# Performance work log

Hardware: AMD Instinct MI355X
Metric: run time of the kernel (lower is better)

Reference implementation:

```python
import jax, jax.numpy as jnp
import numpy as np

G, NPG = 256, 128          # graphs per batch, nodes per graph
N = G * NPG                # 32768 total nodes
E = 524288                 # total directed edges; first half 'in', second half 'out'
DIN, D = 128, 256          # input feature dim, hidden dim
R = 200                    # num relations
C = 2                      # num classes
EPS = 1e-5                 # batchnorm eps


def setup_inputs() -> dict:
    key = jax.random.key(0)
    ks = jax.random.split(key, 20)

    def w(k, shape):
        fan_in = shape[-2] if len(shape) >= 2 else shape[-1]
        return jax.random.normal(k, shape, jnp.float32) / np.float32(np.sqrt(fan_in))

    return {
        "x": jax.random.normal(ks[0], (N, DIN), jnp.float32),
        "rel_emb": w(ks[1], (R, DIN)),
        # conv1: DIN -> D
        "w_in1": w(ks[2], (DIN, D)), "w_out1": w(ks[3], (DIN, D)),
        "w_loop1": w(ks[4], (DIN, D)), "w_rel1": w(ks[5], (DIN, D)),
        "loop_rel1": w(ks[6], (1, DIN)),
        "bias1": jnp.zeros((D,), jnp.float32),
        "gamma1": jnp.ones((D,), jnp.float32), "beta1": jnp.zeros((D,), jnp.float32),
        # conv2..conv5 stacked: D -> D
        "W_in": w(ks[7], (4, D, D)), "W_out": w(ks[8], (4, D, D)),
        "W_loop": w(ks[9], (4, D, D)), "W_rel": w(ks[10], (4, D, D)),
        "Loop_rel": w(ks[11], (4, 1, D)),
        "Bias": jnp.zeros((4, D), jnp.float32),
        "Gamma": jnp.ones((4, D), jnp.float32), "Beta": jnp.zeros((4, D), jnp.float32),
        # head: concat2 => Linear(4*D, C)
        "lin_w": w(ks[12], (4 * D, C)), "lin_b": jnp.zeros((C,), jnp.float32),
        # graph data (int constants)
        "edge_index": jax.random.randint(ks[13], (2, E), 0, N),
        "edge_type": jax.random.randint(ks[14], (E,), 0, R),
        "batch": jnp.repeat(jnp.arange(G, dtype=jnp.int32), NPG),
        "rel_labels": jax.random.randint(ks[15], (G,), 0, R),
    }


def _compgcn_conv(x, rel, edge_index, edge_type,
                  w_in, w_out, w_loop, w_rel, loop_rel, bias, gamma, beta):
    """One CompGCNConv layer (opn='mult', dropout=identity/eval, BN with batch stats)."""
    n = x.shape[0]
    half = edge_index.shape[1] // 2

    def direction(idx, etype, W):
        src, dst = idx[0], idx[1]
        # symmetric normalization: deg^{-1/2}[src] * deg^{-1/2}[dst]
        deg = jax.ops.segment_sum(jnp.ones_like(src, jnp.float32), src, num_segments=n)
        dinv = jnp.where(deg > 0, deg ** -0.5, 0.0)
        norm = dinv[src] * dinv[dst]                       # [half]
        msg = ((x[src] * rel[etype]) @ W) * norm[:, None]  # [half, D]
        return jax.ops.segment_sum(msg, dst, num_segments=n)

    in_res = direction(edge_index[:, :half], edge_type[:half], w_in)
    out_res = direction(edge_index[:, half:], edge_type[half:], w_out)
    loop_res = (x * loop_rel) @ w_loop                     # self-loop, loop relation, no norm

    out = (in_res + out_res + loop_res) / 3.0 + bias
    mean = out.mean(axis=0)
    var = out.var(axis=0)
    out = (out - mean) / jnp.sqrt(var + EPS) * gamma + beta
    return jax.nn.relu(out), rel @ w_rel


def reference(x, rel_emb, w_in1, w_out1, w_loop1, w_rel1, loop_rel1, bias1, gamma1, beta1,
              W_in, W_out, W_loop, W_rel, Loop_rel, Bias, Gamma, Beta,
              lin_w, lin_b, edge_index, edge_type, batch, rel_labels):
    x, r = _compgcn_conv(x, rel_emb, edge_index, edge_type,
                         w_in1, w_out1, w_loop1, w_rel1, loop_rel1, bias1, gamma1, beta1)
    for l in range(4):  # conv2..conv5 (fixed small layer loop)
        x, r = _compgcn_conv(x, r, edge_index, edge_type,
                             W_in[l], W_out[l], W_loop[l], W_rel[l],
                             Loop_rel[l], Bias[l], Gamma[l], Beta[l])

    # per-graph head/tail nodes (first two nodes of each graph) via segment offsets
    counts = jax.ops.segment_sum(jnp.ones((x.shape[0],), jnp.float32), batch, num_segments=G)
    offsets = (jnp.cumsum(counts) - counts).astype(jnp.int32)
    h_batch = x[offsets]
    t_batch = x[offsets + 1]

    pooled = jax.ops.segment_sum(x, batch, num_segments=G) / counts[:, None]
    rel_embs = r[rel_labels]

    feats = jnp.concatenate([pooled, rel_embs, h_batch, t_batch], axis=1)  # concat2 path
    return feats @ lin_w + lin_b


if __name__ == "__main__":
    out = reference(**setup_inputs())
    print(out.shape, out.dtype)
```

## Files before the change

kernel.cpp:

```cpp
#include <hip/hip_runtime.h>

#define NN 32768
#define GG 256
#define NPGN 128
#define ET 524288
#define EH 262144
#define D1 128
#define D2 256
#define RR 200

typedef unsigned short u16;
typedef __attribute__((ext_vector_type(8))) short bf16x8;
typedef __attribute__((ext_vector_type(4))) float f32x4;
typedef __attribute__((ext_vector_type(8))) unsigned short u16x8;
typedef __attribute__((ext_vector_type(4))) unsigned short u16x4;

__device__ __forceinline__ float bf2f(u16 u) {
    union { unsigned int i; float f; } v; v.i = ((unsigned int)u) << 16; return v.f;
}
__device__ __forceinline__ u16 f2bf(float f) {
    union { unsigned int i; float f; } v; v.f = f;
    unsigned int x = v.i;
    return (u16)((x + 0x7fffu + ((x >> 16) & 1u)) >> 16);
}

__global__ void k_hist(const int* __restrict__ ei, int* __restrict__ hs_in,
                       int* __restrict__ hs_out, int* __restrict__ hd_in,
                       int* __restrict__ hd_out) {
    int e = blockIdx.x * blockDim.x + threadIdx.x;
    if (e >= ET) return;
    int s = ei[e], d = ei[ET + e];
    if (e < EH) { atomicAdd(&hs_in[s], 1);  atomicAdd(&hd_in[d], 1); }
    else        { atomicAdd(&hs_out[s], 1); atomicAdd(&hd_out[d], 1); }
}

__global__ void k_dinv(const int* __restrict__ hs_in, const int* __restrict__ hs_out,
                       float* __restrict__ dinv_in, float* __restrict__ dinv_out) {
    int n = blockIdx.x * blockDim.x + threadIdx.x;
    if (n >= NN) return;
    int a = hs_in[n], b = hs_out[n];
    dinv_in[n]  = a > 0 ? rsqrtf((float)a) : 0.f;
    dinv_out[n] = b > 0 ? rsqrtf((float)b) : 0.f;
}

__global__ __launch_bounds__(1024) void k_scan(const int* __restrict__ hist,
                                               int* __restrict__ off) {
    __shared__ int lds[1024];
    int t = threadIdx.x;
    int base = t * 32;
    int loc[32];
    int s = 0;
#pragma unroll
    for (int i = 0; i < 32; ++i) { loc[i] = s; s += hist[base + i]; }
    lds[t] = s;
    int tot = s;
    __syncthreads();
    for (int st = 1; st < 1024; st <<= 1) {
        int v = (t >= st) ? lds[t - st] : 0;
        __syncthreads();
        lds[t] += v;
        __syncthreads();
    }
    int excl = lds[t] - tot;
#pragma unroll
    for (int i = 0; i < 32; ++i) off[base + i] = excl + loc[i];
    if (t == 1023) off[NN] = lds[1023];
}

__global__ void k_fill(const int* __restrict__ ei, const int* __restrict__ et,
                       const float* __restrict__ dinv, const int* __restrict__ off,
                       int* __restrict__ cur, int* __restrict__ c_src,
                       int* __restrict__ c_et, float* __restrict__ c_norm, int eoff) {
    int e = blockIdx.x * blockDim.x + threadIdx.x;
    if (e >= EH) return;
    int s = ei[eoff + e], d = ei[ET + eoff + e], t = et[eoff + e];
    int slot = off[d] + atomicAdd(&cur[d], 1);
    c_src[slot] = s;
    c_et[slot] = t;
    c_norm[slot] = dinv[s] * dinv[d];
}

__global__ void k_convx(const float* __restrict__ in, u16* __restrict__ out, int n) {
    int i = blockIdx.x * blockDim.x + threadIdx.x;
    if (i < n) out[i] = f2bf(in[i]);
}

__global__ void k_prepw(const float* __restrict__ Wi, const float* __restrict__ Wo,
                        const float* __restrict__ Wl, const float* __restrict__ lr,
                        u16* __restrict__ WiT, u16* __restrict__ WoT,
                        u16* __restrict__ WlT, int K, int L) {
    int idx = blockIdx.x * blockDim.x + threadIdx.x;
    int per = L * K * 256;
    if (idx >= 3 * per) return;
    int fam = idx / per, rem = idx % per;
    int l = rem / (K * 256), rr = rem % (K * 256);
    int k = rr / 256, n = rr % 256;
    const float* src = fam == 0 ? Wi : fam == 1 ? Wo : Wl;
    float v = src[((size_t)l * K + k) * 256 + n];
    if (fam == 2) v *= lr[l * K + k];
    u16* dst = fam == 0 ? WiT : fam == 1 ? WoT : WlT;
    dst[((size_t)l * 256 + n) * K + k] = f2bf(v);
}

template <int K>
__global__ __launch_bounds__(256) void k_gather2(
    const u16* __restrict__ x, const u16* __restrict__ relb,
    const int* __restrict__ csI, const int* __restrict__ cetI,
    const float* __restrict__ cnI, const int* __restrict__ offI,
    const int* __restrict__ csO, const int* __restrict__ cetO,
    const float* __restrict__ cnO, const int* __restrict__ offO,
    u16* __restrict__ aggI, u16* __restrict__ aggO) {
    constexpr int VEC = K / 32;
    const int dir = blockIdx.y;
    const int* __restrict__ cs  = dir ? csO : csI;
    const int* __restrict__ cet = dir ? cetO : cetI;
    const float* __restrict__ cn = dir ? cnO : cnI;
    const int* __restrict__ off = dir ? offO : offI;
    u16* __restrict__ agg = dir ? aggO : aggI;

    int node = blockIdx.x * 8 + (threadIdx.x >> 5);
    int l = threadIdx.x & 31;
    int c = l * VEC;
    int e0 = off[node], e1 = off[node + 1];
    float acc[VEC] = {};
    int e = e0;
    for (; e + 2 <= e1; e += 2) {
        int s0 = cs[e],     t0 = cet[e];     float n0 = cn[e];
        int s1 = cs[e + 1], t1 = cet[e + 1]; float n1 = cn[e + 1];
        if constexpr (VEC == 8) {
            u16x8 x0 = *(const u16x8*)(x + (size_t)s0 * K + c);
            u16x8 r0 = *(const u16x8*)(relb + (size_t)t0 * K + c);
            u16x8 x1 = *(const u16x8*)(x + (size_t)s1 * K + c);
            u16x8 r1 = *(const u16x8*)(relb + (size_t)t1 * K + c);
#pragma unroll
            for (int i = 0; i < 8; ++i)
                acc[i] += n0 * bf2f(x0[i]) * bf2f(r0[i]) + n1 * bf2f(x1[i]) * bf2f(r1[i]);
        } else {
            u16x4 x0 = *(const u16x4*)(x + (size_t)s0 * K + c);
            u16x4 r0 = *(const u16x4*)(relb + (size_t)t0 * K + c);
            u16x4 x1 = *(const u16x4*)(x + (size_t)s1 * K + c);
            u16x4 r1 = *(const u16x4*)(relb + (size_t)t1 * K + c);
#pragma unroll
            for (int i = 0; i < 4; ++i)
                acc[i] += n0 * bf2f(x0[i]) * bf2f(r0[i]) + n1 * bf2f(x1[i]) * bf2f(r1[i]);
        }
    }
    if (e < e1) {
        int s0 = cs[e], t0 = cet[e]; float n0 = cn[e];
        if constexpr (VEC == 8) {
            u16x8 x0 = *(const u16x8*)(x + (size_t)s0 * K + c);
            u16x8 r0 = *(const u16x8*)(relb + (size_t)t0 * K + c);
#pragma unroll
            for (int i = 0; i < 8; ++i) acc[i] += n0 * bf2f(x0[i]) * bf2f(r0[i]);
        } else {
            u16x4 x0 = *(const u16x4*)(x + (size_t)s0 * K + c);
            u16x4 r0 = *(const u16x4*)(relb + (size_t)t0 * K + c);
#pragma unroll
            for (int i = 0; i < 4; ++i) acc[i] += n0 * bf2f(x0[i]) * bf2f(r0[i]);
        }
    }
    if constexpr (VEC == 8) {
        u16x8 o;
#pragma unroll
        for (int i = 0; i < 8; ++i) o[i] = f2bf(acc[i]);
        *(u16x8*)(agg + (size_t)node * K + c) = o;
    } else {
        u16x4 o;
#pragma unroll
        for (int i = 0; i < 4; ++i) o[i] = f2bf(acc[i]);
        *(u16x4*)(agg + (size_t)node * K + c) = o;
    }
}

template <int K>
__global__ __launch_bounds__(256) void k_gemm_mfma(
    const u16* __restrict__ A1, const u16* __restrict__ A2, const u16* __restrict__ A3,
    const u16* __restrict__ W1, const u16* __restrict__ W2, const u16* __restrict__ W3,
    const float* __restrict__ bias, float* __restrict__ C, float* __restrict__ bnsums) {
    const int tid = threadIdx.x;
    const int wave = tid >> 6, lane = tid & 63;
    const int q = lane >> 4, r = lane & 15;
    const int rowBase = blockIdx.x * 128 + (wave & 1) * 64;
    const int colBase = blockIdx.y * 128 + (wave >> 1) * 64;
    f32x4 zero = {0.f, 0.f, 0.f, 0.f};
    f32x4 acc[4][4];
#pragma unroll
    for (int i = 0; i < 4; ++i)
#pragma unroll
        for (int j = 0; j < 4; ++j) acc[i][j] = zero;

    const u16* As[3] = {A1, A2, A3};
    const u16* Ws[3] = {W1, W2, W3};
    constexpr int SPS = K / 32;
    constexpr int TOT = 3 * SPS;

    bf16x8 aC[4], bC[4], aN[4], bN[4];
#pragma unroll
    for (int t = 0; t < 4; ++t) {
        aC[t] = *(const bf16x8*)(As[0] + (size_t)(rowBase + t * 16 + r) * K + q * 8);
        bC[t] = *(const bf16x8*)(Ws[0] + (size_t)(colBase + t * 16 + r) * K + q * 8);
    }
#pragma unroll
    for (int s = 0; s < TOT; ++s) {
        if (s + 1 < TOT) {
            const u16* A = As[(s + 1) / SPS];
            const u16* W = Ws[(s + 1) / SPS];
            const int kb = ((s + 1) % SPS) * 32 + q * 8;
#pragma unroll
            for (int t = 0; t < 4; ++t) {
                aN[t] = *(const bf16x8*)(A + (size_t)(rowBase + t * 16 + r) * K + kb);
                bN[t] = *(const bf16x8*)(W + (size_t)(colBase + t * 16 + r) * K + kb);
            }
        }
#pragma unroll
        for (int tm = 0; tm < 4; ++tm)
#pragma unroll
            for (int tn = 0; tn < 4; ++tn)
                acc[tm][tn] = __builtin_amdgcn_mfma_f32_16x16x32_bf16(
                    aC[tm], bC[tn], acc[tm][tn], 0, 0, 0);
#pragma unroll
        for (int t = 0; t < 4; ++t) { aC[t] = aN[t]; bC[t] = bN[t]; }
    }

#pragma unroll
    for (int tn = 0; tn < 4; ++tn) {
        int col = colBase + tn * 16 + r;
        float bv = bias[col];
        float sv = 0.f, qv = 0.f;
#pragma unroll
        for (int tm = 0; tm < 4; ++tm) {
#pragma unroll
            for (int reg = 0; reg < 4; ++reg) {
                int row = rowBase + tm * 16 + q * 4 + reg;
                float v = acc[tm][tn][reg] / 3.0f + bv;
                C[(size_t)row * 256 + col] = v;
                sv += v; qv += v * v;
            }
        }
        sv += __shfl_xor(sv, 16); sv += __shfl_xor(sv, 32);
        qv += __shfl_xor(qv, 16); qv += __shfl_xor(qv, 32);
        if (q == 0) {
            atomicAdd(&bnsums[col], sv);
            atomicAdd(&bnsums[256 + col], qv);
        }
    }
}

__global__ __launch_bounds__(256) void k_gemm_rel(
    const float* __restrict__ A, const float* __restrict__ W,
    float* __restrict__ C, u16* __restrict__ Cb, int M, int K) {
    __shared__ float As[16][68];
    __shared__ float Wshm[16][68];
    const int tid = threadIdx.x;
    const int tx = tid & 15, ty = tid >> 4;
    const int arow = tid >> 2;
    const int akc  = (tid & 3) << 2;
    const int wk   = tid >> 4;
    const int wn0  = (tid & 15) << 2;
    const int rowBase = blockIdx.x << 6;
    const int colBase = blockIdx.y << 6;
    float acc[4][4] = {};
    for (int k0 = 0; k0 < K; k0 += 16) {
        float4 av = make_float4(0.f, 0.f, 0.f, 0.f);
        int rr = rowBase + arow;
        if (rr < M) av = *(const float4*)(A + (size_t)rr * K + k0 + akc);
        As[akc + 0][arow] = av.x;
        As[akc + 1][arow] = av.y;
        As[akc + 2][arow] = av.z;
        As[akc + 3][arow] = av.w;
        float4 wv = *(const float4*)(W + (size_t)(k0 + wk) * D2 + colBase + wn0);
        Wshm[wk][wn0 + 0] = wv.x;
        Wshm[wk][wn0 + 1] = wv.y;
        Wshm[wk][wn0 + 2] = wv.z;
        Wshm[wk][wn0 + 3] = wv.w;
        __syncthreads();
#pragma unroll
        for (int kk = 0; kk < 16; ++kk) {
            float a0 = As[kk][(ty << 2) + 0], a1 = As[kk][(ty << 2) + 1];
            float a2 = As[kk][(ty << 2) + 2], a3 = As[kk][(ty << 2) + 3];
            float w0 = Wshm[kk][(tx << 2) + 0], w1 = Wshm[kk][(tx << 2) + 1];
            float w2 = Wshm[kk][(tx << 2) + 2], w3 = Wshm[kk][(tx << 2) + 3];
            acc[0][0] += a0 * w0; acc[0][1] += a0 * w1; acc[0][2] += a0 * w2; acc[0][3] += a0 * w3;
            acc[1][0] += a1 * w0; acc[1][1] += a1 * w1; acc[1][2] += a1 * w2; acc[1][3] += a1 * w3;
            acc[2][0] += a2 * w0; acc[2][1] += a2 * w1; acc[2][2] += a2 * w2; acc[2][3] += a2 * w3;
            acc[3][0] += a3 * w0; acc[3][1] += a3 * w1; acc[3][2] += a3 * w2; acc[3][3] += a3 * w3;
        }
        __syncthreads();
    }
#pragma unroll
    for (int i = 0; i < 4; ++i) {
        int rr = rowBase + (ty << 2) + i;
        if (rr >= M) continue;
        float* cp = C + (size_t)rr * D2 + colBase + (tx << 2);
        u16* cb = Cb + (size_t)rr * D2 + colBase + (tx << 2);
        cp[0] = acc[i][0]; cp[1] = acc[i][1]; cp[2] = acc[i][2]; cp[3] = acc[i][3];
        cb[0] = f2bf(acc[i][0]); cb[1] = f2bf(acc[i][1]);
        cb[2] = f2bf(acc[i][2]); cb[3] = f2bf(acc[i][3]);
    }
}

__global__ void k_bnapply(const float4* __restrict__ h4, const float* __restrict__ sums,
                          const float* __restrict__ gamma, const float* __restrict__ beta,
                          u16x4* __restrict__ xb4) {
    int idx = blockIdx.x * blockDim.x + threadIdx.x;
    int f0 = (idx & 63) << 2;
    float4 v = h4[idx];
    u16x4 o;
    float vv[4] = {v.x, v.y, v.z, v.w};
#pragma unroll
    for (int i = 0; i < 4; ++i) {
        int f = f0 + i;
        float mean = sums[f] * (1.0f / NN);
        float var  = sums[256 + f] * (1.0f / NN) - mean * mean;
        float inv  = 1.0f / sqrtf(var + 1e-5f);
        float t = (vv[i] - mean) * inv * gamma[f] + beta[f];
        o[i] = f2bf(t > 0.f ? t : 0.f);
    }
    xb4[idx] = o;
}

__global__ void k_feats(const u16* __restrict__ x, const float* __restrict__ rel,
                        const int* __restrict__ rel_labels, float* __restrict__ feats) {
    int g = blockIdx.x, f = threadIdx.x;
    const u16* xg = x + (size_t)g * NPGN * D2;
    float s = 0.f;
#pragma unroll 8
    for (int n = 0; n < NPGN; ++n) s += bf2f(xg[(size_t)n * D2 + f]);
    float* fg = feats + (size_t)g * 1024;
    fg[f]       = s * (1.0f / NPGN);
    fg[256 + f] = rel[(size_t)rel_labels[g] * D2 + f];
    fg[512 + f] = bf2f(xg[f]);
    fg[768 + f] = bf2f(xg[D2 + f]);
}

__global__ void k_head(const float* __restrict__ feats, const float* __restrict__ lw,
                       const float* __restrict__ lb, float* __restrict__ out) {
    int g = blockIdx.x, t = threadIdx.x;
    __shared__ float s0[256], s1[256];
    float a0 = 0.f, a1 = 0.f;
#pragma unroll
    for (int j = 0; j < 4; ++j) {
        int k = t * 4 + j;
        float fv = feats[(size_t)g * 1024 + k];
        a0 += fv * lw[k * 2 + 0];
        a1 += fv * lw[k * 2 + 1];
    }
    s0[t] = a0; s1[t] = a1;
    __syncthreads();
    for (int s = 128; s > 0; s >>= 1) {
        if (t < s) { s0[t] += s0[t + s]; s1[t] += s1[t + s]; }
        __syncthreads();
    }
    if (t == 0) {
        out[g * 2 + 0] = s0[0] + lb[0];
        out[g * 2 + 1] = s1[0] + lb[1];
    }
}

extern "C" void kernel_launch(void* const* d_in, const int* in_sizes, int n_in,
                              void* d_out, int out_size, void* d_ws, size_t ws_size,
                              hipStream_t stream) {
    const float* x0   = (const float*)d_in[0];
    const float* rel0 = (const float*)d_in[1];
    const int* edge_index = (const int*)d_in[20];
    const int* edge_type  = (const int*)d_in[21];
    const int* rel_labels = (const int*)d_in[23];
    float* out = (float*)d_out;

    float* ws = (float*)d_ws;
    float* h     = ws;
    float* relA  = h + (size_t)NN * 256;
    float* relB  = relA + (size_t)RR * 256;
    float* dinv_in  = relB + (size_t)RR * 256;
    float* dinv_out = dinv_in + NN;
    float* cnorm_in  = dinv_out + NN;
    float* cnorm_out = cnorm_in + EH;
    float* bnsums    = cnorm_out + EH;
    float* feats     = bnsums + 512;
    int* csrc_in  = (int*)(feats + GG * 1024);
    int* cet_in   = csrc_in + EH;
    int* csrc_out = cet_in + EH;
    int* cet_out  = csrc_out + EH;
    int* off_in   = cet_out + EH;
    int* off_out  = off_in + NN + 8;
    int* hs_in    = off_out + NN + 8;
    int* hs_out   = hs_in + NN;
    int* hd_in    = hs_out + NN;
    int* hd_out   = hd_in + NN;
    int* cur_in   = hd_out + NN;
    int* cur_out  = cur_in + NN;
    u16* xbf0 = (u16*)(cur_out + NN);
    u16* xbfA = xbf0 + (size_t)NN * 128;
    u16* aggI = xbfA + (size_t)NN * 256;
    u16* aggO = aggI + (size_t)NN * 256;
    u16* wt0  = aggO + (size_t)NN * 256;
    u16* wtS  = wt0 + 3 * 256 * 128;
    u16* relbf = wtS + 12 * 65536;

    hipMemsetAsync(hs_in, 0, 6 * NN * sizeof(int), stream);
    k_hist<<<ET / 256, 256, 0, stream>>>(edge_index, hs_in, hs_out, hd_in, hd_out);
    k_dinv<<<NN / 256, 256, 0, stream>>>(hs_in, hs_out, dinv_in, dinv_out);
    k_scan<<<1, 1024, 0, stream>>>(hd_in, off_in);
    k_scan<<<1, 1024, 0, stream>>>(hd_out, off_out);
    k_fill<<<EH / 256, 256, 0, stream>>>(edge_index, edge_type, dinv_in, off_in,
                                         cur_in, csrc_in, cet_in, cnorm_in, 0);
    k_fill<<<EH / 256, 256, 0, stream>>>(edge_index, edge_type, dinv_out, off_out,
                                         cur_out, csrc_out, cet_out, cnorm_out, EH);
    k_convx<<<(NN * D1) / 256, 256, 0, stream>>>(x0, xbf0, NN * D1);
    k_convx<<<(RR * D1 + 255) / 256, 256, 0, stream>>>(rel0, relbf, RR * D1);
    k_prepw<<<(3 * D1 * 256) / 256, 256, 0, stream>>>(
        (const float*)d_in[2], (const float*)d_in[3], (const float*)d_in[4],
        (const float*)d_in[6], wt0, wt0 + 256 * D1, wt0 + 2 * 256 * D1, D1, 1);
    k_prepw<<<(3 * 4 * D2 * 256) / 256, 256, 0, stream>>>(
        (const float*)d_in[10], (const float*)d_in[11], (const float*)d_in[12],
        (const float*)d_in[14], wtS, wtS + 4 * 65536, wtS + 8 * 65536, D2, 4);

    const float* rc = rel0; float* rn = relA;

    for (int l = 0; l < 5; ++l) {
        const int K = (l == 0) ? D1 : D2;
        const u16* xb = (l == 0) ? xbf0 : xbfA;
        const u16 *WiT, *WoT, *WlT;
        const float *Wr, *bias, *gamma, *beta;
        if (l == 0) {
            WiT = wt0; WoT = wt0 + 256 * D1; WlT = wt0 + 2 * 256 * D1;
            Wr = (const float*)d_in[5];
            bias  = (const float*)d_in[7];
            gamma = (const float*)d_in[8];
            beta  = (const float*)d_in[9];
        } else {
            int m = l - 1;
            WiT = wtS + (size_t)m * 65536;
            WoT = wtS + (size_t)(4 + m) * 65536;
            WlT = wtS + (size_t)(8 + m) * 65536;
            Wr = (const float*)d_in[13] + (size_t)m * D2 * D2;
            bias  = (const float*)d_in[15] + (size_t)m * D2;
            gamma = (const float*)d_in[16] + (size_t)m * D2;
            beta  = (const float*)d_in[17] + (size_t)m * D2;
        }

        dim3 ggr(NN / 8, 2);
        if (K == D1) k_gather2<D1><<<ggr, 256, 0, stream>>>(xb, relbf, csrc_in, cet_in,
            cnorm_in, off_in, csrc_out, cet_out, cnorm_out, off_out, aggI, aggO);
        else         k_gather2<D2><<<ggr, 256, 0, stream>>>(xb, relbf, csrc_in, cet_in,
            cnorm_in, off_in, csrc_out, cet_out, cnorm_out, off_out, aggI, aggO);
        hipMemsetAsync(bnsums, 0, 512 * sizeof(float), stream);
        dim3 ggrid(NN / 128, 2);
        if (K == D1) k_gemm_mfma<D1><<<ggrid, 256, 0, stream>>>(aggI, aggO, xb, WiT, WoT, WlT, bias, h, bnsums);
        else         k_gemm_mfma<D2><<<ggrid, 256, 0, stream>>>(aggI, aggO, xb, WiT, WoT, WlT, bias, h, bnsums);
        k_bnapply<<<(NN * 256 / 4) / 256, 256, 0, stream>>>((const float4*)h, bnsums,
                                                            gamma, beta, (u16x4*)xbfA);
        k_gemm_rel<<<dim3(4, 4), 256, 0, stream>>>(rc, Wr, rn, relbf, RR, K);
        const float* nr = rn;
        rn = (l == 0) ? relB : (float*)rc;
        rc = nr;
    }

    k_feats<<<GG, 256, 0, stream>>>(xbfA, rc, rel_labels, feats);
    k_head<<<GG, 256, 0, stream>>>(feats, (const float*)d_in[18],
                                   (const float*)d_in[19], out);
}
```

Baseline: 925.8 us.

## Stage GEMM tiles through LDS with async loads and widen gather edges

The MFMA GEMM now stages 128x32 A and W tiles into double-buffered shared memory using global_load_lds, rather than each wave loading its fragments directly from global memory. This lets waves in a block reuse the same tile data and cuts redundant global traffic. The gather kernel now uses 8-wide bf16 vectors for both hidden sizes (16 nodes per block for K=128) and processes 4 edges per iteration to raise memory-level parallelism. The risks are a __syncthreads per k-step, which can stall while async loads are still in flight, and higher register pressure in the gather loop.

```diff
diff --git a/kernel.cpp b/kernel.cpp
--- a/kernel.cpp
+++ b/kernel.cpp
@@ -110,7 +110,8 @@
     const int* __restrict__ csO, const int* __restrict__ cetO,
     const float* __restrict__ cnO, const int* __restrict__ offO,
     u16* __restrict__ aggI, u16* __restrict__ aggO) {
-    constexpr int VEC = K / 32;
+    constexpr int LPN = K / 8;
+    constexpr int NPB = 256 / LPN;
     const int dir = blockIdx.y;
     const int* __restrict__ cs  = dir ? csO : csI;
     const int* __restrict__ cet = dir ? cetO : cetI;
@@ -118,57 +119,53 @@
     const int* __restrict__ off = dir ? offO : offI;
     u16* __restrict__ agg = dir ? aggO : aggI;
 
-    int node = blockIdx.x * 8 + (threadIdx.x >> 5);
-    int l = threadIdx.x & 31;
-    int c = l * VEC;
+    int node = blockIdx.x * NPB + (threadIdx.x / LPN);
+    int lane = threadIdx.x % LPN;
+    int c = lane * 8;
     int e0 = off[node], e1 = off[node + 1];
-    float acc[VEC] = {};
+    float acc[8] = {};
     int e = e0;
-    for (; e + 2 <= e1; e += 2) {
-        int s0 = cs[e],     t0 = cet[e];     float n0 = cn[e];
-        int s1 = cs[e + 1], t1 = cet[e + 1]; float n1 = cn[e + 1];
-        if constexpr (VEC == 8) {
-            u16x8 x0 = *(const u16x8*)(x + (size_t)s0 * K + c);
-            u16x8 r0 = *(const u16x8*)(relb + (size_t)t0 * K + c);
-            u16x8 x1 = *(const u16x8*)(x + (size_t)s1 * K + c);
-            u16x8 r1 = *(const u16x8*)(relb + (size_t)t1 * K + c);
-#pragma unroll
-            for (int i = 0; i < 8; ++i)
-                acc[i] += n0 * bf2f(x0[i]) * bf2f(r0[i]) + n1 * bf2f(x1[i]) * bf2f(r1[i]);
-        } else {
-            u16x4 x0 = *(const u16x4*)(x + (size_t)s0 * K + c);
-            u16x4 r0 = *(const u16x4*)(relb + (size_t)t0 * K + c);
-            u16x4 x1 = *(const u16x4*)(x + (size_t)s1 * K + c);
-            u16x4 r1 = *(const u16x4*)(relb + (size_t)t1 * K + c);
-#pragma unroll
-            for (int i = 0; i < 4; ++i)
-                acc[i] += n0 * bf2f(x0[i]) * bf2f(r0[i]) + n1 * bf2f(x1[i]) * bf2f(r1[i]);
-        }
-    }
-    if (e < e1) {
+    for (; e + 4 <= e1; e += 4) {
+        int s0 = cs[e],     s1 = cs[e + 1], s2 = cs[e + 2], s3 = cs[e + 3];
+        int t0 = cet[e],    t1 = cet[e + 1], t2 = cet[e + 2], t3 = cet[e + 3];
+        float n0 = cn[e], n1 = cn[e + 1], n2 = cn[e + 2], n3 = cn[e + 3];
+        u16x8 xa = *(const u16x8*)(x + (size_t)s0 * K + c);
+        u16x8 xb = *(const u16x8*)(x + (size_t)s1 * K + c);
+        u16x8 xc = *(const u16x8*)(x + (size_t)s2 * K + c);
+        u16x8 xd = *(const u16x8*)(x + (size_t)s3 * K + c);
+        u16x8 ra = *(const u16x8*)(relb + (size_t)t0 * K + c);
+        u16x8 rb = *(const u16x8*)(relb + (size_t)t1 * K + c);
+        u16x8 rc = *(const u16x8*)(relb + (size_t)t2 * K + c);
+        u16x8 rd = *(const u16x8*)(relb + (size_t)t3 * K + c);
+#pragma unroll
+        for (int i = 0; i < 8; ++i)
+            acc[i] += n0 * bf2f(xa[i]) * bf2f(ra[i]) + n1 * bf2f(xb[i]) * bf2f(rb[i])
+                    + n2 * bf2f(xc[i]) * bf2f(rc[i]) + n3 * bf2f(xd[i]) * bf2f(rd[i]);
+    }
+    for (; e < e1; ++e) {
         int s0 = cs[e], t0 = cet[e]; float n0 = cn[e];
-        if constexpr (VEC == 8) {
-            u16x8 x0 = *(const u16x8*)(x + (size_t)s0 * K + c);
-            u16x8 r0 = *(const u16x8*)(relb + (size_t)t0 * K + c);
-#pragma unroll
-            for (int i = 0; i < 8; ++i) acc[i] += n0 * bf2f(x0[i]) * bf2f(r0[i]);
-        } else {
-            u16x4 x0 = *(const u16x4*)(x + (size_t)s0 * K + c);
-            u16x4 r0 = *(const u16x4*)(relb + (size_t)t0 * K + c);
-#pragma unroll
-            for (int i = 0; i < 4; ++i) acc[i] += n0 * bf2f(x0[i]) * bf2f(r0[i]);
-        }
-    }
-    if constexpr (VEC == 8) {
-        u16x8 o;
-#pragma unroll
-        for (int i = 0; i < 8; ++i) o[i] = f2bf(acc[i]);
-        *(u16x8*)(agg + (size_t)node * K + c) = o;
-    } else {
-        u16x4 o;
-#pragma unroll
-        for (int i = 0; i < 4; ++i) o[i] = f2bf(acc[i]);
-        *(u16x4*)(agg + (size_t)node * K + c) = o;
+        u16x8 xa = *(const u16x8*)(x + (size_t)s0 * K + c);
+        u16x8 ra = *(const u16x8*)(relb + (size_t)t0 * K + c);
+#pragma unroll
+        for (int i = 0; i < 8; ++i) acc[i] += n0 * bf2f(xa[i]) * bf2f(ra[i]);
+    }
+    u16x8 o;
+#pragma unroll
+    for (int i = 0; i < 8; ++i) o[i] = f2bf(acc[i]);
+    *(u16x8*)(agg + (size_t)node * K + c) = o;
+}
+
+__device__ __forceinline__ void stage_tile(const u16* __restrict__ src, int baseRow,
+                                           int K, int kk, u16* lds, int wave, int lane) {
+#pragma unroll
+    for (int i = 0; i < 2; ++i) {
+        int chunk = wave * 2 + i;
+        int row = chunk * 16 + (lane >> 2);
+        const u16* g = src + (size_t)(baseRow + row) * K + kk + (lane & 3) * 8;
+        u16* l = lds + chunk * 512;
+        __builtin_amdgcn_global_load_lds((const __attribute__((address_space(1))) void*)g,
+                                         (__attribute__((address_space(3))) void*)l,
+                                         16, 0, 0);
     }
 }
 
@@ -177,11 +174,16 @@
     const u16* __restrict__ A1, const u16* __restrict__ A2, const u16* __restrict__ A3,
     const u16* __restrict__ W1, const u16* __restrict__ W2, const u16* __restrict__ W3,
     const float* __restrict__ bias, float* __restrict__ C, float* __restrict__ bnsums) {
+    __shared__ u16 As_s[2][128 * 32];
+    __shared__ u16 Ws_s[2][128 * 32];
     const int tid = threadIdx.x;
     const int wave = tid >> 6, lane = tid & 63;
     const int q = lane >> 4, r = lane & 15;
-    const int rowBase = blockIdx.x * 128 + (wave & 1) * 64;
-    const int colBase = blockIdx.y * 128 + (wave >> 1) * 64;
+    const int rowBlk = blockIdx.x * 128;
+    const int colBlk = blockIdx.y * 128;
+    const int rowBase = rowBlk + (wave & 1) * 64;
+    const int colBase = colBlk + (wave >> 1) * 64;
+
     f32x4 zero = {0.f, 0.f, 0.f, 0.f};
     f32x4 acc[4][4];
 #pragma unroll
@@ -194,32 +196,31 @@
     constexpr int SPS = K / 32;
     constexpr int TOT = 3 * SPS;
 
-    bf16x8 aC[4], bC[4], aN[4], bN[4];
-#pragma unroll
-    for (int t = 0; t < 4; ++t) {
-        aC[t] = *(const bf16x8*)(As[0] + (size_t)(rowBase + t * 16 + r) * K + q * 8);
-        bC[t] = *(const bf16x8*)(Ws[0] + (size_t)(colBase + t * 16 + r) * K + q * 8);
-    }
-#pragma unroll
+    stage_tile(As[0], rowBlk, K, 0, As_s[0], wave, lane);
+    stage_tile(Ws[0], colBlk, K, 0, Ws_s[0], wave, lane);
+
     for (int s = 0; s < TOT; ++s) {
+        __syncthreads();
         if (s + 1 < TOT) {
-            const u16* A = As[(s + 1) / SPS];
-            const u16* W = Ws[(s + 1) / SPS];
-            const int kb = ((s + 1) % SPS) * 32 + q * 8;
-#pragma unroll
-            for (int t = 0; t < 4; ++t) {
-                aN[t] = *(const bf16x8*)(A + (size_t)(rowBase + t * 16 + r) * K + kb);
-                bN[t] = *(const bf16x8*)(W + (size_t)(colBase + t * 16 + r) * K + kb);
-            }
+            int seg = (s + 1) / SPS;
+            int kk  = ((s + 1) % SPS) * 32;
+            stage_tile(As[seg], rowBlk, K, kk, As_s[(s + 1) & 1], wave, lane);
+            stage_tile(Ws[seg], colBlk, K, kk, Ws_s[(s + 1) & 1], wave, lane);
+        }
+        const u16* al = As_s[s & 1] + (wave & 1) * 64 * 32;
+        const u16* wl = Ws_s[s & 1] + (wave >> 1) * 64 * 32;
+        bf16x8 a[4], b[4];
+#pragma unroll
+        for (int t = 0; t < 4; ++t) {
+            a[t] = *(const bf16x8*)(al + (t * 16 + r) * 32 + q * 8);
+            b[t] = *(const bf16x8*)(wl + (t * 16 + r) * 32 + q * 8);
         }
 #pragma unroll
         for (int tm = 0; tm < 4; ++tm)
 #pragma unroll
             for (int tn = 0; tn < 4; ++tn)
                 acc[tm][tn] = __builtin_amdgcn_mfma_f32_16x16x32_bf16(
-                    aC[tm], bC[tn], acc[tm][tn], 0, 0, 0);
-#pragma unroll
-        for (int t = 0; t < 4; ++t) { aC[t] = aN[t]; bC[t] = bN[t]; }
+                    a[tm], b[tn], acc[tm][tn], 0, 0, 0);
     }
 
 #pragma unroll
@@ -439,11 +440,15 @@
             beta  = (const float*)d_in[17] + (size_t)m * D2;
         }
 
-        dim3 ggr(NN / 8, 2);
-        if (K == D1) k_gather2<D1><<<ggr, 256, 0, stream>>>(xb, relbf, csrc_in, cet_in,
-            cnorm_in, off_in, csrc_out, cet_out, cnorm_out, off_out, aggI, aggO);
-        else         k_gather2<D2><<<ggr, 256, 0, stream>>>(xb, relbf, csrc_in, cet_in,
-            cnorm_in, off_in, csrc_out, cet_out, cnorm_out, off_out, aggI, aggO);
+        if (K == D1) {
+            dim3 ggr(NN / 16, 2);
+            k_gather2<D1><<<ggr, 256, 0, stream>>>(xb, relbf, csrc_in, cet_in,
+                cnorm_in, off_in, csrc_out, cet_out, cnorm_out, off_out, aggI, aggO);
+        } else {
+            dim3 ggr(NN / 8, 2);
+            k_gather2<D2><<<ggr, 256, 0, stream>>>(xb, relbf, csrc_in, cet_in,
+                cnorm_in, off_in, csrc_out, cet_out, cnorm_out, off_out, aggI, aggO);
+        }
         hipMemsetAsync(bnsums, 0, 512 * sizeof(float), stream);
         dim3 ggrid(NN / 128, 2);
         if (K == D1) k_gemm_mfma<D1><<<ggrid, 256, 0, stream>>>(aggI, aggO, xb, WiT, WoT, WlT, bias, h, bnsums);
```

New measurement: 829.5 us. 10.4% less time.
